# Optimization experiments

Measured on AMD Instinct MI355X. Metric: run time of the kernel, lower is better.

Reference implementation:

```python
import jax, jax.numpy as jnp
import numpy as np

N, T, D, H = 64, 1024, 1024, 1024


def setup_inputs() -> dict:
    key = jax.random.key(0)
    k1, k2, k3, k4 = jax.random.split(key, 4)
    x = jax.random.normal(k1, (N, T, D), dtype=jnp.float32)
    h0 = jax.random.normal(k2, (N, H), dtype=jnp.float32)
    Wx = jax.random.normal(k3, (D, 4 * H), dtype=jnp.float32) / np.sqrt(D)
    Wh = jax.random.normal(k4, (H, 4 * H), dtype=jnp.float32) / np.sqrt(H)
    b = jnp.zeros((4 * H,), dtype=jnp.float32)
    return {"x": x, "h0": h0, "Wx": Wx, "Wh": Wh, "b": b}


def reference(x, h0, Wx, Wh, b):
    # Precompute input projection for all timesteps: (N,T,4H)
    xW = jnp.einsum('ntd,dk->ntk', x, Wx) + b
    c0 = jnp.zeros_like(h0)

    def step(carry, xw_t):
        h, c = carry
        A = xw_t + h @ Wh            # (N,4H)
        i, f, o, g = jnp.split(A, 4, axis=-1)
        c_new = jax.nn.sigmoid(f) * c + jax.nn.sigmoid(i) * jnp.tanh(g)
        h_new = jax.nn.sigmoid(o) * jnp.tanh(c_new)
        return (h_new, c_new), h_new

    # scan over time axis: (T,N,4H)
    _, hs = jax.lax.scan(step, (h0, c0), jnp.swapaxes(xW, 0, 1))
    return jnp.swapaxes(hs, 0, 1)     # (N,T,H)
```

## Files before the change

kernel.cpp:

```cpp
#include <hip/hip_runtime.h>
#include <hip/hip_fp16.h>


typedef _Float16 f16x8 __attribute__((ext_vector_type(8)));
typedef _Float16 f16x4 __attribute__((ext_vector_type(4)));
typedef float    f32x4 __attribute__((ext_vector_type(4)));

#define LN 64
#define LT 1024
#define LD 1024
#define LH 1024
#define G4 4096

#define OFF_BAR  ((size_t)0)
#define OFF_H16  ((size_t)4096)
#define OFF_X16  (OFF_H16 + (size_t)2*LN*LH*2)
#define OFF_WXT  (OFF_X16 + (size_t)LN*LT*LD*2)
#define OFF_WHP  (OFF_WXT + (size_t)LD*G4*2)
#define OFF_XW   (OFF_WHP + (size_t)LH*G4*2)
#define WS_NEED  (OFF_XW  + (size_t)LN*LT*G4*2)

__device__ __forceinline__ float fast_sigmoid(float x) {
  float e = __expf(-fabsf(x));
  float s = __fdividef(e, 1.f + e);
  return x >= 0.f ? 1.f - s : s;
}
__device__ __forceinline__ float fast_tanh(float x) {
  float e = __expf(-2.f * fabsf(x));
  float t = __fdividef(1.f - e, 1.f + e);
  return x >= 0.f ? t : -t;
}


__global__ void k_cvt_x(const float* __restrict__ x, _Float16* __restrict__ x16) {
  size_t i = (size_t)blockIdx.x * 256 + threadIdx.x;
  float4 v = ((const float4*)x)[i];
  f16x4 o;
  o[0] = (_Float16)v.x; o[1] = (_Float16)v.y; o[2] = (_Float16)v.z; o[3] = (_Float16)v.w;
  ((f16x4*)x16)[i] = o;
}

__global__ void k_cvt_h0(const float* __restrict__ h0, _Float16* __restrict__ h16) {
  int i = blockIdx.x * 256 + threadIdx.x;
  h16[i] = (_Float16)h0[i];
}

__global__ void k_tr_wx(const float* __restrict__ Wx, _Float16* __restrict__ WxT) {
  __shared__ float tile[64][65];
  const int c0 = blockIdx.x * 64;
  const int d0 = blockIdx.y * 64;
  const int tx = threadIdx.x & 63, ty = threadIdx.x >> 6;
  for (int r = ty; r < 64; r += 4)
    tile[r][tx] = Wx[(size_t)(d0 + r) * G4 + c0 + tx];
  __syncthreads();
  for (int r = ty; r < 64; r += 4)
    WxT[(size_t)(c0 + r) * LD + d0 + tx] = (_Float16)tile[tx][r];
}

__global__ void k_pack_wh(const float* __restrict__ Wh, _Float16* __restrict__ whp) {
  unsigned u = blockIdx.x * 256 + threadIdx.x;
  int lane = u & 63; unsigned r = u >> 6;
  int kc = r & 7; r >>= 3;
  int g  = r & 3; r >>= 2;
  int w  = r & 3;
  int bid = r >> 2;
  int col = g * 1024 + bid * 16 + (lane & 15);
  int k0  = w * 256 + kc * 32 + (lane >> 4) * 8;
  f16x8 v;
#pragma unroll
  for (int j = 0; j < 8; ++j) v[j] = (_Float16)Wh[(size_t)(k0 + j) * G4 + col];
  ((f16x8*)whp)[u] = v;
}


__device__ __forceinline__ void gl_lds16(const _Float16* g, _Float16* l) {
  __builtin_amdgcn_global_load_lds(
      (const __attribute__((address_space(1))) unsigned int*)g,
      (__attribute__((address_space(3))) unsigned int*)l, 16, 0, 0);
}

__global__ __launch_bounds__(256) void k_gemm_xw(const _Float16* __restrict__ A,
                                                 const _Float16* __restrict__ B,
                                                 _Float16* __restrict__ C) {
  __shared__ _Float16 As[128 * 64];
  __shared__ _Float16 Bs[128 * 64];
  const int tid = threadIdx.x;
  const int lane = tid & 63;
  const int w = tid >> 6;
  const int wm = w & 1, wn = w >> 1;
  const int m0 = blockIdx.x * 128;
  const int n0 = blockIdx.y * 128;
  const int lr = lane >> 3;
  const int lcb = (lane & 7) * 8;

  f32x4 acc[4][4];
#pragma unroll
  for (int i = 0; i < 4; ++i)
#pragma unroll
    for (int j = 0; j < 4; ++j) acc[i][j] = (f32x4){0.f, 0.f, 0.f, 0.f};

  for (int kt = 0; kt < 16; ++kt) {
    const int k0 = kt * 64;
#pragma unroll
    for (int c2 = 0; c2 < 4; ++c2) {
      int chunk = w * 4 + c2;
      int row = chunk * 8 + lr;
      gl_lds16(&A[(size_t)(m0 + row) * LD + k0 + lcb], &As[chunk * 512]);
      gl_lds16(&B[(size_t)(n0 + row) * LD + k0 + lcb], &Bs[chunk * 512]);
    }
    __syncthreads();
#pragma unroll
    for (int kc = 0; kc < 2; ++kc) {
      const int ko = kc * 32 + (lane >> 4) * 8;
      f16x8 Af[4], Bf[4];
#pragma unroll
      for (int mt = 0; mt < 4; ++mt)
        Af[mt] = *(const f16x8*)&As[(wm * 64 + mt * 16 + (lane & 15)) * 64 + ko];
#pragma unroll
      for (int nt = 0; nt < 4; ++nt)
        Bf[nt] = *(const f16x8*)&Bs[(wn * 64 + nt * 16 + (lane & 15)) * 64 + ko];
#pragma unroll
      for (int mt = 0; mt < 4; ++mt)
#pragma unroll
        for (int nt = 0; nt < 4; ++nt)
          acc[mt][nt] = __builtin_amdgcn_mfma_f32_16x16x32_f16(Af[mt], Bf[nt], acc[mt][nt], 0, 0, 0);
    }
    __syncthreads();
  }
#pragma unroll
  for (int mt = 0; mt < 4; ++mt) {
#pragma unroll
    for (int nt = 0; nt < 4; ++nt) {
      int col = n0 + wn * 64 + nt * 16 + (lane & 15);
#pragma unroll
      for (int r = 0; r < 4; ++r) {
        int m = m0 + wm * 64 + mt * 16 + (lane >> 4) * 4 + r;
        int n = m >> 10, t = m & 1023;
        C[((size_t)t * 64 + n) * G4 + col] = (_Float16)acc[mt][nt][r];
      }
    }
  }
}


__global__ __launch_bounds__(256, 1) void k_lstm(
    const _Float16* __restrict__ whp, const _Float16* __restrict__ xw,
    const float* __restrict__ bias, _Float16* h16, float* __restrict__ out,
    unsigned int* __restrict__ bar) {
  const int tid = threadIdx.x, bid = blockIdx.x;
  const int lane = tid & 63, w = tid >> 6;
  const int hx = tid & 15, b4 = tid >> 4;
  __shared__ float Ared[4096];

  f16x8 Bf[4][8];
  {
    const f16x8* bp = (const f16x8*)whp + ((size_t)(bid * 4 + w) * 32) * 64 + lane;
#pragma unroll
    for (int g = 0; g < 4; ++g)
#pragma unroll
      for (int kc = 0; kc < 8; ++kc) Bf[g][kc] = bp[(g * 8 + kc) * 64];
  }
  float bv[4];
#pragma unroll
  for (int g = 0; g < 4; ++g) bv[g] = bias[g * 1024 + bid * 16 + hx];
  float cst[4] = {0.f, 0.f, 0.f, 0.f};

  for (int i = tid; i < 1024; i += 256) ((f32x4*)Ared)[i] = (f32x4){0.f, 0.f, 0.f, 0.f};
  __syncthreads();

  const int arow = lane & 15;
  const int kbase = w * 256 + (lane >> 4) * 8;
  int p = 0;

  for (int t = 0; t < LT; ++t) {
    __builtin_amdgcn_fence(__ATOMIC_ACQUIRE, "agent");

    float xwv[4][4];
#pragma unroll
    for (int q = 0; q < 4; ++q)
#pragma unroll
      for (int g = 0; g < 4; ++g)
        xwv[q][g] = (float)xw[((size_t)t * 64 + b4 * 4 + q) * G4 + g * 1024 + bid * 16 + hx];

    const _Float16* hc = h16 + (size_t)p * (LN * LH);
    f32x4 acc[4][4];
#pragma unroll
    for (int i = 0; i < 4; ++i)
#pragma unroll
      for (int j = 0; j < 4; ++j) acc[i][j] = (f32x4){0.f, 0.f, 0.f, 0.f};

#pragma unroll
    for (int kc = 0; kc < 8; ++kc) {
      f16x8 Af[4];
#pragma unroll
      for (int mt = 0; mt < 4; ++mt)
        Af[mt] = *(const f16x8*)&hc[(mt * 16 + arow) * LH + kbase + kc * 32];
#pragma unroll
      for (int mt = 0; mt < 4; ++mt)
#pragma unroll
        for (int g = 0; g < 4; ++g)
          acc[mt][g] = __builtin_amdgcn_mfma_f32_16x16x32_f16(Af[mt], Bf[g][kc], acc[mt][g], 0, 0, 0);
    }

#pragma unroll
    for (int mi = 0; mi < 4; ++mi) {
      int mt = (mi + w) & 3;
#pragma unroll
      for (int gi = 0; gi < 4; ++gi) {
        int g = (gi + w) & 3;
#pragma unroll
        for (int r = 0; r < 4; ++r)
          atomicAdd(&Ared[(mt * 16 + (lane >> 4) * 4 + r) * 64 + g * 16 + (lane & 15)],
                    acc[mt][g][r]);
      }
    }
    __syncthreads();

    _Float16* hn = h16 + (size_t)(p ^ 1) * (LN * LH);
#pragma unroll
    for (int q = 0; q < 4; ++q) {
      const int b = b4 * 4 + q;
      float Ai = Ared[b * 64 +  0 + hx] + xwv[q][0] + bv[0];
      float Af_ = Ared[b * 64 + 16 + hx] + xwv[q][1] + bv[1];
      float Ao = Ared[b * 64 + 32 + hx] + xwv[q][2] + bv[2];
      float Ag = Ared[b * 64 + 48 + hx] + xwv[q][3] + bv[3];
      float iv = fast_sigmoid(Ai), fv = fast_sigmoid(Af_), ov = fast_sigmoid(Ao);
      float gv = fast_tanh(Ag);
      float cn = fv * cst[q] + iv * gv;
      cst[q] = cn;
      float hv = ov * fast_tanh(cn);
      union { _Float16 h; unsigned short u; } cvt; cvt.h = (_Float16)hv;
      __hip_atomic_store((unsigned short*)&hn[b * 1024 + bid * 16 + hx], cvt.u,
                         __ATOMIC_RELAXED, __HIP_MEMORY_SCOPE_AGENT);
      __builtin_nontemporal_store(hv, &out[((size_t)b * 1024 + t) * 1024 + bid * 16 + hx]);
    }
    __syncthreads();

    if (tid == 0)
      __hip_atomic_fetch_add(bar, 1u, __ATOMIC_RELAXED, __HIP_MEMORY_SCOPE_AGENT);

    for (int i = tid; i < 1024; i += 256) ((f32x4*)Ared)[i] = (f32x4){0.f, 0.f, 0.f, 0.f};
    __syncthreads();

    if (tid == 0) {
      const unsigned tgt = 64u * (t + 1);
      while (__hip_atomic_load(bar, __ATOMIC_RELAXED, __HIP_MEMORY_SCOPE_AGENT) < tgt)
        __builtin_amdgcn_s_sleep(8);
    }
    __syncthreads();
    p ^= 1;
  }
}


extern "C" void kernel_launch(void* const* d_in, const int* in_sizes, int n_in,
                              void* d_out, int out_size, void* d_ws, size_t ws_size,
                              hipStream_t stream) {
  const float* x  = (const float*)d_in[0];
  const float* h0 = (const float*)d_in[1];
  const float* Wx = (const float*)d_in[2];
  const float* Wh = (const float*)d_in[3];
  const float* b  = (const float*)d_in[4];
  float* out = (float*)d_out;
  char* ws = (char*)d_ws;
  if (ws_size < WS_NEED) return;

  unsigned int* bar = (unsigned int*)(ws + OFF_BAR);
  _Float16* h16 = (_Float16*)(ws + OFF_H16);
  _Float16* x16 = (_Float16*)(ws + OFF_X16);
  _Float16* wxT = (_Float16*)(ws + OFF_WXT);
  _Float16* whp = (_Float16*)(ws + OFF_WHP);
  _Float16* xw  = (_Float16*)(ws + OFF_XW);

  hipMemsetAsync(bar, 0, 256, stream);
  hipLaunchKernelGGL(k_cvt_x,   dim3(65536),   dim3(256), 0, stream, x, x16);
  hipLaunchKernelGGL(k_cvt_h0,  dim3(256),     dim3(256), 0, stream, h0, h16);
  hipLaunchKernelGGL(k_tr_wx,   dim3(64, 16),  dim3(256), 0, stream, Wx, wxT);
  hipLaunchKernelGGL(k_pack_wh, dim3(2048),    dim3(256), 0, stream, Wh, whp);
  hipLaunchKernelGGL(k_gemm_xw, dim3(512, 32), dim3(256), 0, stream, x16, wxT, xw);
  hipLaunchKernelGGL(k_lstm,    dim3(64),      dim3(256), 0, stream, whp, xw, b, h16, out, bar);
}
```

Measured before the change: 32.65 ms.

## Replace atomic-counter grid barrier with per-block flags and vectorize gate epilogue

Result: slower. 37.78 ms (+15.7%).

```diff
diff --git a/kernel.cpp b/kernel.cpp
--- a/kernel.cpp
+++ b/kernel.cpp
@@ -13,12 +13,14 @@
 #define G4 4096
 
 #define OFF_BAR  ((size_t)0)
-#define OFF_H16  ((size_t)4096)
+#define OFF_H16  ((size_t)8192)
 #define OFF_X16  (OFF_H16 + (size_t)2*LN*LH*2)
 #define OFF_WXT  (OFF_X16 + (size_t)LN*LT*LD*2)
 #define OFF_WHP  (OFF_WXT + (size_t)LD*G4*2)
 #define OFF_XW   (OFF_WHP + (size_t)LH*G4*2)
 #define WS_NEED  (OFF_XW  + (size_t)LN*LT*G4*2)
+
+#define ARS 68
 
 __device__ __forceinline__ float fast_sigmoid(float x) {
   float e = __expf(-fabsf(x));
@@ -146,11 +148,11 @@
 __global__ __launch_bounds__(256, 1) void k_lstm(
     const _Float16* __restrict__ whp, const _Float16* __restrict__ xw,
     const float* __restrict__ bias, _Float16* h16, float* __restrict__ out,
-    unsigned int* __restrict__ bar) {
+    unsigned int* __restrict__ flags) {
   const int tid = threadIdx.x, bid = blockIdx.x;
   const int lane = tid & 63, w = tid >> 6;
-  const int hx = tid & 15, b4 = tid >> 4;
-  __shared__ float Ared[4096];
+  const int gb = tid >> 2, gq = tid & 3;
+  __shared__ float Ared[64 * ARS];
 
   f16x8 Bf[4][8];
   {
@@ -160,27 +162,34 @@
 #pragma unroll
       for (int kc = 0; kc < 8; ++kc) Bf[g][kc] = bp[(g * 8 + kc) * 64];
   }
-  float bv[4];
-#pragma unroll
-  for (int g = 0; g < 4; ++g) bv[g] = bias[g * 1024 + bid * 16 + hx];
+  f32x4 bvv[4];
+#pragma unroll
+  for (int g = 0; g < 4; ++g)
+    bvv[g] = *(const f32x4*)&bias[g * 1024 + bid * 16 + gq * 4];
   float cst[4] = {0.f, 0.f, 0.f, 0.f};
 
-  for (int i = tid; i < 1024; i += 256) ((f32x4*)Ared)[i] = (f32x4){0.f, 0.f, 0.f, 0.f};
-  __syncthreads();
+  for (int i = tid; i < (64 * ARS) / 4; i += 256) ((f32x4*)Ared)[i] = (f32x4){0.f, 0.f, 0.f, 0.f};
 
   const int arow = lane & 15;
   const int kbase = w * 256 + (lane >> 4) * 8;
   int p = 0;
 
   for (int t = 0; t < LT; ++t) {
+    f16x4 xwv[4];
+    {
+      const _Float16* xwp = xw + ((size_t)t * 64 + gb) * G4 + bid * 16 + gq * 4;
+#pragma unroll
+      for (int g = 0; g < 4; ++g) xwv[g] = *(const f16x4*)&xwp[(size_t)g * 1024];
+    }
+
+    if (t) {
+      const unsigned want = (unsigned)t;
+      while (__any(__hip_atomic_load(&flags[lane * 32], __ATOMIC_RELAXED,
+                                     __HIP_MEMORY_SCOPE_AGENT) < want))
+        __builtin_amdgcn_s_sleep(1);
+    }
+    __syncthreads();
     __builtin_amdgcn_fence(__ATOMIC_ACQUIRE, "agent");
-
-    float xwv[4][4];
-#pragma unroll
-    for (int q = 0; q < 4; ++q)
-#pragma unroll
-      for (int g = 0; g < 4; ++g)
-        xwv[q][g] = (float)xw[((size_t)t * 64 + b4 * 4 + q) * G4 + g * 1024 + bid * 16 + hx];
 
     const _Float16* hc = h16 + (size_t)p * (LN * LH);
     f32x4 acc[4][4];
@@ -189,18 +198,32 @@
 #pragma unroll
       for (int j = 0; j < 4; ++j) acc[i][j] = (f32x4){0.f, 0.f, 0.f, 0.f};
 
-#pragma unroll
-    for (int kc = 0; kc < 8; ++kc) {
-      f16x8 Af[4];
-#pragma unroll
-      for (int mt = 0; mt < 4; ++mt)
-        Af[mt] = *(const f16x8*)&hc[(mt * 16 + arow) * LH + kbase + kc * 32];
-#pragma unroll
-      for (int mt = 0; mt < 4; ++mt)
-#pragma unroll
-        for (int g = 0; g < 4; ++g)
-          acc[mt][g] = __builtin_amdgcn_mfma_f32_16x16x32_f16(Af[mt], Bf[g][kc], acc[mt][g], 0, 0, 0);
-    }
+#define LDH(kc, mt) (*(const f16x8*)&hc[((mt) * 16 + arow) * LH + kbase + (kc) * 32])
+    {
+      f16x8 Afa[4], Afb[4];
+#pragma unroll
+      for (int mt = 0; mt < 4; ++mt) Afa[mt] = LDH(0, mt);
+#pragma unroll
+      for (int kp = 0; kp < 4; ++kp) {
+#pragma unroll
+        for (int mt = 0; mt < 4; ++mt) Afb[mt] = LDH(2 * kp + 1, mt);
+#pragma unroll
+        for (int mt = 0; mt < 4; ++mt)
+#pragma unroll
+          for (int g = 0; g < 4; ++g)
+            acc[mt][g] = __builtin_amdgcn_mfma_f32_16x16x32_f16(Afa[mt], Bf[g][2 * kp], acc[mt][g], 0, 0, 0);
+        if (kp < 3) {
+#pragma unroll
+          for (int mt = 0; mt < 4; ++mt) Afa[mt] = LDH(2 * kp + 2, mt);
+        }
+#pragma unroll
+        for (int mt = 0; mt < 4; ++mt)
+#pragma unroll
+          for (int g = 0; g < 4; ++g)
+            acc[mt][g] = __builtin_amdgcn_mfma_f32_16x16x32_f16(Afb[mt], Bf[g][2 * kp + 1], acc[mt][g], 0, 0, 0);
+      }
+    }
+#undef LDH
 
 #pragma unroll
     for (int mi = 0; mi < 4; ++mi) {
@@ -210,44 +233,50 @@
         int g = (gi + w) & 3;
 #pragma unroll
         for (int r = 0; r < 4; ++r)
-          atomicAdd(&Ared[(mt * 16 + (lane >> 4) * 4 + r) * 64 + g * 16 + (lane & 15)],
+          atomicAdd(&Ared[(mt * 16 + (lane >> 4) * 4 + r) * ARS + g * 16 + (lane & 15)],
                     acc[mt][g][r]);
       }
     }
     __syncthreads();
 
     _Float16* hn = h16 + (size_t)(p ^ 1) * (LN * LH);
-#pragma unroll
-    for (int q = 0; q < 4; ++q) {
-      const int b = b4 * 4 + q;
-      float Ai = Ared[b * 64 +  0 + hx] + xwv[q][0] + bv[0];
-      float Af_ = Ared[b * 64 + 16 + hx] + xwv[q][1] + bv[1];
-      float Ao = Ared[b * 64 + 32 + hx] + xwv[q][2] + bv[2];
-      float Ag = Ared[b * 64 + 48 + hx] + xwv[q][3] + bv[3];
-      float iv = fast_sigmoid(Ai), fv = fast_sigmoid(Af_), ov = fast_sigmoid(Ao);
-      float gv = fast_tanh(Ag);
-      float cn = fv * cst[q] + iv * gv;
-      cst[q] = cn;
-      float hv = ov * fast_tanh(cn);
-      union { _Float16 h; unsigned short u; } cvt; cvt.h = (_Float16)hv;
-      __hip_atomic_store((unsigned short*)&hn[b * 1024 + bid * 16 + hx], cvt.u,
+    {
+      f32x4 Ag[4];
+#pragma unroll
+      for (int g = 0; g < 4; ++g) {
+        f32x4 r = *(const f32x4*)&Ared[gb * ARS + g * 16 + gq * 4];
+        f32x4 xf;
+#pragma unroll
+        for (int j = 0; j < 4; ++j) xf[j] = (float)xwv[g][j];
+        Ag[g] = r + xf + bvv[g];
+      }
+      f16x4 hv4;
+      f32x4 o4;
+#pragma unroll
+      for (int j = 0; j < 4; ++j) {
+        float iv = fast_sigmoid(Ag[0][j]);
+        float fv = fast_sigmoid(Ag[1][j]);
+        float ov = fast_sigmoid(Ag[2][j]);
+        float gv = fast_tanh(Ag[3][j]);
+        float cn = fv * cst[j] + iv * gv;
+        cst[j] = cn;
+        float hv = ov * fast_tanh(cn);
+        hv4[j] = (_Float16)hv;
+        o4[j] = hv;
+      }
+      union { f16x4 v; unsigned long long u; } cvt;
+      cvt.v = hv4;
+      __hip_atomic_store((unsigned long long*)&hn[gb * 1024 + bid * 16 + gq * 4], cvt.u,
                          __ATOMIC_RELAXED, __HIP_MEMORY_SCOPE_AGENT);
-      __builtin_nontemporal_store(hv, &out[((size_t)b * 1024 + t) * 1024 + bid * 16 + hx]);
+      __builtin_nontemporal_store(o4, (f32x4*)&out[((size_t)gb * 1024 + t) * 1024 + bid * 16 + gq * 4]);
     }
     __syncthreads();
 
     if (tid == 0)
-      __hip_atomic_fetch_add(bar, 1u, __ATOMIC_RELAXED, __HIP_MEMORY_SCOPE_AGENT);
-
-    for (int i = tid; i < 1024; i += 256) ((f32x4*)Ared)[i] = (f32x4){0.f, 0.f, 0.f, 0.f};
-    __syncthreads();
-
-    if (tid == 0) {
-      const unsigned tgt = 64u * (t + 1);
-      while (__hip_atomic_load(bar, __ATOMIC_RELAXED, __HIP_MEMORY_SCOPE_AGENT) < tgt)
-        __builtin_amdgcn_s_sleep(8);
-    }
-    __syncthreads();
+      __hip_atomic_store(&flags[bid * 32], (unsigned)(t + 1), __ATOMIC_RELEASE,
+                         __HIP_MEMORY_SCOPE_AGENT);
+
+    for (int i = tid; i < (64 * ARS) / 4; i += 256) ((f32x4*)Ared)[i] = (f32x4){0.f, 0.f, 0.f, 0.f};
     p ^= 1;
   }
 }
@@ -265,18 +294,18 @@
   char* ws = (char*)d_ws;
   if (ws_size < WS_NEED) return;
 
-  unsigned int* bar = (unsigned int*)(ws + OFF_BAR);
+  unsigned int* flags = (unsigned int*)(ws + OFF_BAR);
   _Float16* h16 = (_Float16*)(ws + OFF_H16);
   _Float16* x16 = (_Float16*)(ws + OFF_X16);
   _Float16* wxT = (_Float16*)(ws + OFF_WXT);
   _Float16* whp = (_Float16*)(ws + OFF_WHP);
   _Float16* xw  = (_Float16*)(ws + OFF_XW);
 
-  hipMemsetAsync(bar, 0, 256, stream);
+  hipMemsetAsync(flags, 0, 8192, stream);
   hipLaunchKernelGGL(k_cvt_x,   dim3(65536),   dim3(256), 0, stream, x, x16);
   hipLaunchKernelGGL(k_cvt_h0,  dim3(256),     dim3(256), 0, stream, h0, h16);
   hipLaunchKernelGGL(k_tr_wx,   dim3(64, 16),  dim3(256), 0, stream, Wx, wxT);
   hipLaunchKernelGGL(k_pack_wh, dim3(2048),    dim3(256), 0, stream, Wh, whp);
   hipLaunchKernelGGL(k_gemm_xw, dim3(512, 32), dim3(256), 0, stream, x16, wxT, xw);
-  hipLaunchKernelGGL(k_lstm,    dim3(64),      dim3(256), 0, stream, whp, xw, b, h16, out, bar);
-}
+  hipLaunchKernelGGL(k_lstm,    dim3(64),      dim3(256), 0, stream, whp, xw, b, h16, out, flags);
+}
```
